# Optimization experiments

Measured on AMD Instinct MI355X. Metric: run time of the kernel, lower is better.

Reference implementation:

```python
import jax, jax.numpy as jnp
import numpy as np

N = 50000
E_RAND = 800000
IN, HID, OUT = 128, 64, 40
HEADS = (2, 1, 1)
NEG_SLOPE = 0.2


def setup_inputs() -> dict:
    key = jax.random.key(0)
    ks = jax.random.split(key, 16)
    # random edges with src != dst, then append self-loops (remove+add_self_loop)
    src_r = jax.random.randint(ks[0], (E_RAND,), 0, N)
    off = jax.random.randint(ks[1], (E_RAND,), 1, N)
    dst_r = (src_r + off) % N
    loops = jnp.arange(N)
    src = jnp.concatenate([src_r, loops]).astype(jnp.int64)
    dst = jnp.concatenate([dst_r, loops]).astype(jnp.int64)
    in_feat = jax.random.normal(ks[2], (N, IN), dtype=jnp.float32)

    def lin(k, fan_in, fan_out):
        return jax.random.normal(k, (fan_in, fan_out), dtype=jnp.float32) / np.sqrt(fan_in)

    H0, H1, H2 = HEADS
    # layer 0: in=IN, out=HID, heads=H0
    W0 = lin(ks[3], IN, H0 * HID)
    al0 = jax.random.normal(ks[4], (H0, HID), dtype=jnp.float32) * 0.1
    ar0 = jax.random.normal(ks[5], (H0, HID), dtype=jnp.float32) * 0.1
    b0 = jnp.zeros((H0 * HID,), dtype=jnp.float32)
    # layer 1: in=HID*H0, out=HID, heads=H1
    W1 = lin(ks[6], HID * H0, H1 * HID)
    al1 = jax.random.normal(ks[7], (H1, HID), dtype=jnp.float32) * 0.1
    ar1 = jax.random.normal(ks[8], (H1, HID), dtype=jnp.float32) * 0.1
    b1 = jnp.zeros((H1 * HID,), dtype=jnp.float32)
    # layer 2: in=HID*H1, out=OUT, heads=H2
    W2 = lin(ks[9], HID * H1, H2 * OUT)
    al2 = jax.random.normal(ks[10], (H2, OUT), dtype=jnp.float32) * 0.1
    ar2 = jax.random.normal(ks[11], (H2, OUT), dtype=jnp.float32) * 0.1
    b2 = jnp.zeros((H2 * OUT,), dtype=jnp.float32)
    return {"in_feat": in_feat, "src": src, "dst": dst,
            "W0": W0, "al0": al0, "ar0": ar0, "b0": b0,
            "W1": W1, "al1": al1, "ar1": ar1, "b1": b1,
            "W2": W2, "al2": al2, "ar2": ar2, "b2": b2}


def _gat_layer(x, src, dst, W, al, ar, b):
    # x: [N, Fin]; W: [Fin, H*D]; al/ar: [H, D]; b: [H*D]
    H, D = al.shape
    feat = (x @ W).reshape(-1, H, D)                 # [N, H, D]
    el = jnp.sum(feat * al, axis=-1)                 # [N, H]
    er = jnp.sum(feat * ar, axis=-1)                 # [N, H]
    e = jax.nn.leaky_relu(el[src] + er[dst], NEG_SLOPE)  # [E, H]
    m = jax.ops.segment_max(e, dst, num_segments=x.shape[0])
    ee = jnp.exp(e - jax.lax.stop_gradient(m)[dst])
    s = jax.ops.segment_sum(ee, dst, num_segments=x.shape[0])
    alpha = ee / s[dst]                              # softmax over in-edges per dst
    out = jax.ops.segment_sum(feat[src] * alpha[:, :, None], dst,
                              num_segments=x.shape[0])  # [N, H, D]
    return out + b.reshape(1, H, D)


def reference(in_feat, src, dst, W0, al0, ar0, b0, W1, al1, ar1, b1, W2, al2, ar2, b2):
    h = _gat_layer(in_feat, src, dst, W0, al0, ar0, b0).reshape(in_feat.shape[0], -1)  # flatten(1)
    h = _gat_layer(h, src, dst, W1, al1, ar1, b1).mean(axis=1)                          # mean over heads
    h = _gat_layer(h, src, dst, W2, al2, ar2, b2).reshape(in_feat.shape[0], -1)         # flatten(1)
    return h
```

## Files before the change

kernel.cpp:

```cpp
#include <hip/hip_runtime.h>
#include <hip/hip_fp16.h>
#include <math.h>

#define NEG_SLOPE 0.2f


__device__ inline float2 up2(unsigned u) {
    __half2 h;
    __builtin_memcpy(&h, &u, 4);
    return __half22float2(h);
}
__device__ inline unsigned pk2(float a, float b) {
    __half2 h = __floats2half2_rn(a, b);
    unsigned u;
    __builtin_memcpy(&u, &h, 4);
    return u;
}
__device__ inline void fma8(float* acc, const uint4& v, float p) {
    float2 f;
    f = up2(v.x); acc[0] += f.x * p; acc[1] += f.y * p;
    f = up2(v.y); acc[2] += f.x * p; acc[3] += f.y * p;
    f = up2(v.z); acc[4] += f.x * p; acc[5] += f.y * p;
    f = up2(v.w); acc[6] += f.x * p; acc[7] += f.y * p;
}
__device__ inline void fma4(float4& a, const float4& w, float xs) {
    a.x += w.x * xs; a.y += w.y * xs; a.z += w.z * xs; a.w += w.w * xs;
}
__device__ inline float dot4(const float4& a, const float4& b) {
    return a.x * b.x + a.y * b.y + a.z * b.z + a.w * b.w;
}


__global__ __launch_bounds__(256) void degree_hist_rank(const int* __restrict__ dst,
                                                        int* __restrict__ deg,
                                                        int* __restrict__ rank, int E) {
    int e = blockIdx.x * blockDim.x + threadIdx.x;
    if (e < E) rank[e] = atomicAdd(&deg[dst[e]], 1);
}

__global__ __launch_bounds__(256) void scan_block_sums(const int* __restrict__ in,
                                                       int* __restrict__ partial, int n) {
    int i = blockIdx.x * 256 + threadIdx.x;
    int v = (i < n) ? in[i] : 0;
#pragma unroll
    for (int off = 32; off; off >>= 1) v += __shfl_xor(v, off);
    __shared__ int wsum[4];
    if ((threadIdx.x & 63) == 0) wsum[threadIdx.x >> 6] = v;
    __syncthreads();
    if (threadIdx.x == 0) partial[blockIdx.x] = wsum[0] + wsum[1] + wsum[2] + wsum[3];
}

__global__ __launch_bounds__(256) void scan_offsets(const int* __restrict__ partial,
                                                    int* __restrict__ partial_scan,
                                                    int* __restrict__ total_out, int nb,
                                                    const float* __restrict__ W2,
                                                    const float* __restrict__ al2,
                                                    const float* __restrict__ ar2,
                                                    float* __restrict__ W2p,
                                                    float* __restrict__ al2p,
                                                    float* __restrict__ ar2p) {
    __shared__ int buf[256];
    int t = threadIdx.x;
    int v = (t < nb) ? partial[t] : 0;
    buf[t] = v;
    __syncthreads();
    for (int off = 1; off < 256; off <<= 1) {
        int x = (t >= off) ? buf[t - off] : 0;
        __syncthreads();
        buf[t] += x;
        __syncthreads();
    }
    partial_scan[t] = buf[t] - v;
    if (t == 255) *total_out = buf[255];
    for (int i = t; i < 64 * 64; i += 256) {
        int r = i >> 6, c = i & 63;
        W2p[i] = (c < 40) ? W2[r * 40 + c] : 0.f;
    }
    if (t < 64) {
        al2p[t] = (t < 40) ? al2[t] : 0.f;
        ar2p[t] = (t < 40) ? ar2[t] : 0.f;
    }
}

__global__ __launch_bounds__(256) void scan_final(const int* __restrict__ in,
                                                  const int* __restrict__ partial_scan,
                                                  int* __restrict__ out, int n) {
    __shared__ int buf[256];
    int t = threadIdx.x;
    int i = blockIdx.x * 256 + t;
    int v = (i < n) ? in[i] : 0;
    buf[t] = v;
    __syncthreads();
    for (int off = 1; off < 256; off <<= 1) {
        int x = (t >= off) ? buf[t - off] : 0;
        __syncthreads();
        buf[t] += x;
        __syncthreads();
    }
    if (i < n) out[i] = partial_scan[blockIdx.x] + buf[t] - v;
}

__global__ __launch_bounds__(256) void scatter_rank(const int* __restrict__ src,
                                                    const int* __restrict__ dst,
                                                    const int* __restrict__ rank,
                                                    const int* __restrict__ row_start,
                                                    int* __restrict__ csr_src, int E) {
    int e = blockIdx.x * blockDim.x + threadIdx.x;
    if (e >= E) return;
    int d = dst[e];
    csr_src[row_start[d] + rank[e]] = src[e];
}


template <int K, int M, int G, int RPG, int H, int FSTRIDE>
__global__ __launch_bounds__((M / 4) * G) void gemm_feat_lds(const float* __restrict__ x,
                                                             const float* __restrict__ W,
                                                             const float* __restrict__ al,
                                                             const float* __restrict__ ar,
                                                             __half* __restrict__ outh,
                                                             float* __restrict__ el,
                                                             float* __restrict__ er, int N) {
    constexpr int CT = M / 4;
    constexpr int NT = CT * G;
    constexpr int ROWS = G * RPG;
    constexpr int KC = 32;
    constexpr int KC4 = KC / 4;
    constexpr int NCH = K / KC;
    constexpr int LPH = 16;
    static_assert(CT % LPH == 0, "CT must be a multiple of 16");
    __shared__ float4 sx[ROWS][KC4 + 1];
    __shared__ float4 sw[KC][CT];
    const int tid = threadIdx.x;
    const int col4 = tid % CT;
    const int grp = tid / CT;
    const int h = col4 / LPH;
    const float4* __restrict__ W4 = (const float4*)W;
    const float4* __restrict__ x4 = (const float4*)x;
    const float4 av = ((const float4*)al)[col4];
    const float4 rv = ((const float4*)ar)[col4];

    for (int base = blockIdx.x * ROWS; base < N; base += gridDim.x * ROWS) {
        float4 acc[RPG];
#pragma unroll
        for (int rr = 0; rr < RPG; ++rr) acc[rr] = float4{0.f, 0.f, 0.f, 0.f};

        for (int ch = 0; ch < NCH; ++ch) {
            __syncthreads();
#pragma unroll
            for (int i = tid; i < KC * CT; i += NT)
                sw[i / CT][i % CT] = W4[(size_t)(ch * KC) * CT + i];
#pragma unroll
            for (int i = tid; i < ROWS * KC4; i += NT) {
                int r = i / KC4, c = i % KC4;
                int row = base + r;
                sx[r][c] = (row < N) ? x4[(size_t)row * (K / 4) + ch * KC4 + c]
                                     : float4{0.f, 0.f, 0.f, 0.f};
            }
            __syncthreads();
#pragma unroll
            for (int k4 = 0; k4 < KC4; ++k4) {
                float4 w0 = sw[4 * k4 + 0][col4];
                float4 w1 = sw[4 * k4 + 1][col4];
                float4 w2 = sw[4 * k4 + 2][col4];
                float4 w3 = sw[4 * k4 + 3][col4];
#pragma unroll
                for (int rr = 0; rr < RPG; ++rr) {
                    float4 xv = sx[grp * RPG + rr][k4];
                    fma4(acc[rr], w0, xv.x);
                    fma4(acc[rr], w1, xv.y);
                    fma4(acc[rr], w2, xv.z);
                    fma4(acc[rr], w3, xv.w);
                }
            }
        }
#pragma unroll
        for (int rr = 0; rr < RPG; ++rr) {
            int row = base + grp * RPG + rr;
            if (row < N) {
                uint2 pkd;
                pkd.x = pk2(acc[rr].x, acc[rr].y);
                pkd.y = pk2(acc[rr].z, acc[rr].w);
                ((uint2*)(outh + (size_t)row * FSTRIDE))[col4] = pkd;
            }
        }
#pragma unroll
        for (int rr = 0; rr < RPG; ++rr) {
            float pl = dot4(acc[rr], av);
            float pr = dot4(acc[rr], rv);
#pragma unroll
            for (int off = 1; off < LPH; off <<= 1) {
                pl += __shfl_xor(pl, off);
                pr += __shfl_xor(pr, off);
            }
            if ((col4 % LPH) == 0) {
                int row = base + grp * RPG + rr;
                if (row < N) {
                    el[(size_t)row * H + h] = pl;
                    er[(size_t)row * H + h] = pr;
                }
            }
        }
    }
}


template <int H, int D, int FSTRIDE, int T>
__global__ __launch_bounds__(256) void gat_aggregate(const __half* __restrict__ feat,
                                                     const float* __restrict__ el,
                                                     const float* __restrict__ er,
                                                     const int* __restrict__ row_start,
                                                     const int* __restrict__ csr_src,
                                                     const float* __restrict__ bias,
                                                     float* __restrict__ out, int N) {
    constexpr int NLp = FSTRIDE / 8;
    constexpr int Gn = 64 / NLp;
    constexpr int BATCH = Gn * T;
    constexpr int WL = (H * D) / 8;
    static_assert(BATCH <= 64 && 64 % NLp == 0, "layout");
    int dstn = (blockIdx.x * blockDim.x + threadIdx.x) >> 6;
    int lane = threadIdx.x & 63;
    if (dstn >= N) return;
    int beg = row_start[dstn], end = row_start[dstn + 1];
    int cnt = end - beg;

    float er_d[H];
#pragma unroll
    for (int h = 0; h < H; ++h) er_d[h] = er[(size_t)dstn * H + h];

    float ssum[H];
    float acc8[8];
#pragma unroll
    for (int h = 0; h < H; ++h) ssum[h] = 0.f;
#pragma unroll
    for (int i = 0; i < 8; ++i) acc8[i] = 0.f;

    const int g = lane / NLp;
    const int ln = lane % NLp;

    auto gather = [&](int s_reg, const float p_reg[H], int j) {
        uint4 v[T];
#pragma unroll
        for (int t = 0; t < T; ++t) {
            int sj = __shfl(s_reg, j + Gn * t + g);
            v[t] = ((const uint4*)(feat + (size_t)sj * FSTRIDE))[ln];
        }
#pragma unroll
        for (int t = 0; t < T; ++t) {
            int slot = j + Gn * t + g;
            float pj = __shfl(p_reg[0], slot);
            if constexpr (H == 2) {
                float pj1 = __shfl(p_reg[1], slot);
                pj = (ln >= 8) ? pj1 : pj;
            }
            fma8(acc8, v[t], pj);
        }
    };

    if (cnt <= 64) {
        int idx = beg + lane;
        bool valid = idx < end;
        int s = valid ? csr_src[idx] : csr_src[beg];
        float ev[H], m[H], p[H];
        if constexpr (H == 2) {
            float2 e2 = ((const float2*)el)[s];
            ev[0] = e2.x + er_d[0];
            ev[1] = e2.y + er_d[1];
        } else {
            ev[0] = el[s] + er_d[0];
        }
#pragma unroll
        for (int h = 0; h < H; ++h) {
            float e = ev[h];
            e = (e > 0.f) ? e : NEG_SLOPE * e;
            ev[h] = e;
            m[h] = valid ? e : -INFINITY;
        }
#pragma unroll
        for (int h = 0; h < H; ++h)
#pragma unroll
            for (int off = 32; off; off >>= 1) m[h] = fmaxf(m[h], __shfl_xor(m[h], off));
#pragma unroll
        for (int h = 0; h < H; ++h) {
            p[h] = valid ? expf(ev[h] - m[h]) : 0.f;
            ssum[h] = p[h];
        }
        for (int j = 0; j < cnt; j += BATCH) gather(s, p, j);
    } else {
        float m[H];
#pragma unroll
        for (int h = 0; h < H; ++h) m[h] = -INFINITY;
        for (int i = beg + lane; i < end; i += 64) {
            int s = csr_src[i];
            float ev[H];
            if constexpr (H == 2) {
                float2 e2 = ((const float2*)el)[s];
                ev[0] = e2.x + er_d[0];
                ev[1] = e2.y + er_d[1];
            } else {
                ev[0] = el[s] + er_d[0];
            }
#pragma unroll
            for (int h = 0; h < H; ++h) {
                float e = ev[h];
                e = (e > 0.f) ? e : NEG_SLOPE * e;
                m[h] = fmaxf(m[h], e);
            }
        }
#pragma unroll
        for (int h = 0; h < H; ++h)
#pragma unroll
            for (int off = 32; off; off >>= 1) m[h] = fmaxf(m[h], __shfl_xor(m[h], off));

        for (int base = beg; base < end; base += 64) {
            int idx = base + lane;
            bool valid = idx < end;
            int s = valid ? csr_src[idx] : csr_src[beg];
            float p[H];
            float ev[H];
            if constexpr (H == 2) {
                float2 e2 = ((const float2*)el)[s];
                ev[0] = e2.x + er_d[0];
                ev[1] = e2.y + er_d[1];
            } else {
                ev[0] = el[s] + er_d[0];
            }
#pragma unroll
            for (int h = 0; h < H; ++h) {
                float e = ev[h];
                e = (e > 0.f) ? e : NEG_SLOPE * e;
                p[h] = valid ? expf(e - m[h]) : 0.f;
                ssum[h] += p[h];
            }
            int ccnt = (end - base < 64) ? end - base : 64;
            for (int j = 0; j < ccnt; j += BATCH) gather(s, p, j);
        }
    }

#pragma unroll
    for (int h = 0; h < H; ++h)
#pragma unroll
        for (int off = 32; off; off >>= 1) ssum[h] += __shfl_xor(ssum[h], off);
#pragma unroll
    for (int i = 0; i < 8; ++i) {
#pragma unroll
        for (int off = NLp; off < 64; off <<= 1) acc8[i] += __shfl_xor(acc8[i], off);
    }
    if (lane < WL) {
        float inv;
        if constexpr (H == 2) inv = 1.f / ((lane >= 8) ? ssum[1] : ssum[0]);
        else inv = 1.f / ssum[0];
        float4* op = (float4*)(out + (size_t)dstn * (H * D));
        const float4* bp = (const float4*)bias;
        float4 bv0 = bp[2 * lane], bv1 = bp[2 * lane + 1];
        float4 o0, o1;
        o0.x = acc8[0] * inv + bv0.x; o0.y = acc8[1] * inv + bv0.y;
        o0.z = acc8[2] * inv + bv0.z; o0.w = acc8[3] * inv + bv0.w;
        o1.x = acc8[4] * inv + bv1.x; o1.y = acc8[5] * inv + bv1.y;
        o1.z = acc8[6] * inv + bv1.z; o1.w = acc8[7] * inv + bv1.w;
        op[2 * lane] = o0;
        op[2 * lane + 1] = o1;
    }
}


extern "C" void kernel_launch(void* const* d_in, const int* in_sizes, int n_in,
                              void* d_out, int out_size, void* d_ws, size_t ws_size,
                              hipStream_t stream) {
    const float* in_feat = (const float*)d_in[0];
    const int*   src     = (const int*)d_in[1];
    const int*   dst     = (const int*)d_in[2];
    const float* W0 = (const float*)d_in[3];
    const float* al0 = (const float*)d_in[4];
    const float* ar0 = (const float*)d_in[5];
    const float* b0 = (const float*)d_in[6];
    const float* W1 = (const float*)d_in[7];
    const float* al1 = (const float*)d_in[8];
    const float* ar1 = (const float*)d_in[9];
    const float* b1 = (const float*)d_in[10];
    const float* W2 = (const float*)d_in[11];
    const float* al2 = (const float*)d_in[12];
    const float* ar2 = (const float*)d_in[13];
    const float* b2 = (const float*)d_in[14];
    float* out = (float*)d_out;

    const int N = in_sizes[0] / 128;
    const int E = in_sizes[1];

    char* ws = (char*)d_ws;
    auto alloc = [&](size_t bytes) -> void* {
        void* p = (void*)ws;
        ws += (bytes + 255) & ~(size_t)255;
        return p;
    };
    int* deg       = (int*)alloc((size_t)N * 4);
    int* row_start = (int*)alloc((size_t)(N + 1) * 4);
    int* csr_src   = (int*)alloc((size_t)E * 4);
    int* rank      = (int*)alloc((size_t)E * 4);
    int* partial      = (int*)alloc(256 * 4);
    int* partial_scan = (int*)alloc(256 * 4);
    __half* feat   = (__half*)alloc((size_t)N * 128 * 2);
    float* el      = (float*)alloc((size_t)N * 2 * 4);
    float* er      = (float*)alloc((size_t)N * 2 * 4);
    float* h0      = (float*)alloc((size_t)N * 128 * 4);
    float* h1      = (float*)alloc((size_t)N * 64 * 4);
    float* W2p     = (float*)alloc((size_t)64 * 64 * 4);
    float* al2p    = (float*)alloc(64 * 4);
    float* ar2p    = (float*)alloc(64 * 4);

    hipMemsetAsync(deg, 0, (size_t)N * 4, stream);

    int egrid = (E + 255) / 256;
    int nb = (N + 255) / 256;

    degree_hist_rank<<<egrid, 256, 0, stream>>>(dst, deg, rank, E);
    scan_block_sums<<<nb, 256, 0, stream>>>(deg, partial, N);
    scan_offsets<<<1, 256, 0, stream>>>(partial, partial_scan, &row_start[N], nb,
                                        W2, al2, ar2, W2p, al2p, ar2p);
    scan_final<<<nb, 256, 0, stream>>>(deg, partial_scan, row_start, N);
    scatter_rank<<<egrid, 256, 0, stream>>>(src, dst, rank, row_start, csr_src, E);

    int ngrid = (N * 64 + 255) / 256;
    int ggrid32 = (N + 31) / 32;
    int ggrid64 = (N + 63) / 64;

    gemm_feat_lds<128, 128, 8, 4, 2, 128><<<ggrid32, 256, 0, stream>>>(in_feat, W0, al0, ar0, feat, el, er, N);
    gat_aggregate<2, 64, 128, 4><<<ngrid, 256, 0, stream>>>(feat, el, er, row_start, csr_src, b0, h0, N);

    gemm_feat_lds<128, 64, 16, 4, 1, 64><<<ggrid64, 256, 0, stream>>>(h0, W1, al1, ar1, feat, el, er, N);
    gat_aggregate<1, 64, 64, 4><<<ngrid, 256, 0, stream>>>(feat, el, er, row_start, csr_src, b1, h1, N);

    gemm_feat_lds<64, 64, 16, 4, 1, 64><<<ggrid64, 256, 0, stream>>>(h1, W2p, al2p, ar2p, feat, el, er, N);
    gat_aggregate<1, 40, 64, 4><<<ngrid, 256, 0, stream>>>(feat, el, er, row_start, csr_src, b2, out, N);
}
```

Before: 311.3 us.

## Drop softmax max-subtraction, use fast exp, guard gather tail, nontemporal CSR loads

```diff
diff --git a/kernel.cpp b/kernel.cpp
--- a/kernel.cpp
+++ b/kernel.cpp
@@ -35,7 +35,10 @@
                                                         int* __restrict__ deg,
                                                         int* __restrict__ rank, int E) {
     int e = blockIdx.x * blockDim.x + threadIdx.x;
-    if (e < E) rank[e] = atomicAdd(&deg[dst[e]], 1);
+    if (e >= E) return;
+    int d = __builtin_nontemporal_load(&dst[e]);
+    int r = atomicAdd(&deg[d], 1);
+    __builtin_nontemporal_store(r, &rank[e]);
 }
 
 __global__ __launch_bounds__(256) void scan_block_sums(const int* __restrict__ in,
@@ -107,8 +110,10 @@
                                                     int* __restrict__ csr_src, int E) {
     int e = blockIdx.x * blockDim.x + threadIdx.x;
     if (e >= E) return;
-    int d = dst[e];
-    csr_src[row_start[d] + rank[e]] = src[e];
+    int d = __builtin_nontemporal_load(&dst[e]);
+    int s = __builtin_nontemporal_load(&src[e]);
+    int r = __builtin_nontemporal_load(&rank[e]);
+    csr_src[row_start[d] + r] = s;
 }
 
 
@@ -237,22 +242,26 @@
     const int g = lane / NLp;
     const int ln = lane % NLp;
 
-    auto gather = [&](int s_reg, const float p_reg[H], int j) {
+    auto gather = [&](int s_reg, const float p_reg[H], int j, int limit) {
         uint4 v[T];
 #pragma unroll
         for (int t = 0; t < T; ++t) {
-            int sj = __shfl(s_reg, j + Gn * t + g);
-            v[t] = ((const uint4*)(feat + (size_t)sj * FSTRIDE))[ln];
+            if (j + Gn * t < limit) {
+                int sj = __shfl(s_reg, j + Gn * t + g);
+                v[t] = ((const uint4*)(feat + (size_t)sj * FSTRIDE))[ln];
+            }
         }
 #pragma unroll
         for (int t = 0; t < T; ++t) {
-            int slot = j + Gn * t + g;
-            float pj = __shfl(p_reg[0], slot);
-            if constexpr (H == 2) {
-                float pj1 = __shfl(p_reg[1], slot);
-                pj = (ln >= 8) ? pj1 : pj;
-            }
-            fma8(acc8, v[t], pj);
+            if (j + Gn * t < limit) {
+                int slot = j + Gn * t + g;
+                float pj = __shfl(p_reg[0], slot);
+                if constexpr (H == 2) {
+                    float pj1 = __shfl(p_reg[1], slot);
+                    pj = (ln >= 8) ? pj1 : pj;
+                }
+                fma8(acc8, v[t], pj);
+            }
         }
     };
 
@@ -260,7 +269,7 @@
         int idx = beg + lane;
         bool valid = idx < end;
         int s = valid ? csr_src[idx] : csr_src[beg];
-        float ev[H], m[H], p[H];
+        float ev[H], p[H];
         if constexpr (H == 2) {
             float2 e2 = ((const float2*)el)[s];
             ev[0] = e2.x + er_d[0];
@@ -272,45 +281,11 @@
         for (int h = 0; h < H; ++h) {
             float e = ev[h];
             e = (e > 0.f) ? e : NEG_SLOPE * e;
-            ev[h] = e;
-            m[h] = valid ? e : -INFINITY;
-        }
-#pragma unroll
-        for (int h = 0; h < H; ++h)
-#pragma unroll
-            for (int off = 32; off; off >>= 1) m[h] = fmaxf(m[h], __shfl_xor(m[h], off));
-#pragma unroll
-        for (int h = 0; h < H; ++h) {
-            p[h] = valid ? expf(ev[h] - m[h]) : 0.f;
+            p[h] = valid ? __expf(e) : 0.f;
             ssum[h] = p[h];
         }
-        for (int j = 0; j < cnt; j += BATCH) gather(s, p, j);
+        for (int j = 0; j < cnt; j += BATCH) gather(s, p, j, cnt);
     } else {
-        float m[H];
-#pragma unroll
-        for (int h = 0; h < H; ++h) m[h] = -INFINITY;
-        for (int i = beg + lane; i < end; i += 64) {
-            int s = csr_src[i];
-            float ev[H];
-            if constexpr (H == 2) {
-                float2 e2 = ((const float2*)el)[s];
-                ev[0] = e2.x + er_d[0];
-                ev[1] = e2.y + er_d[1];
-            } else {
-                ev[0] = el[s] + er_d[0];
-            }
-#pragma unroll
-            for (int h = 0; h < H; ++h) {
-                float e = ev[h];
-                e = (e > 0.f) ? e : NEG_SLOPE * e;
-                m[h] = fmaxf(m[h], e);
-            }
-        }
-#pragma unroll
-        for (int h = 0; h < H; ++h)
-#pragma unroll
-            for (int off = 32; off; off >>= 1) m[h] = fmaxf(m[h], __shfl_xor(m[h], off));
-
         for (int base = beg; base < end; base += 64) {
             int idx = base + lane;
             bool valid = idx < end;
@@ -328,11 +303,11 @@
             for (int h = 0; h < H; ++h) {
                 float e = ev[h];
                 e = (e > 0.f) ? e : NEG_SLOPE * e;
-                p[h] = valid ? expf(e - m[h]) : 0.f;
+                p[h] = valid ? __expf(e) : 0.f;
                 ssum[h] += p[h];
             }
             int ccnt = (end - base < 64) ? end - base : 64;
-            for (int j = 0; j < ccnt; j += BATCH) gather(s, p, j);
+            for (int j = 0; j < ccnt; j += BATCH) gather(s, p, j, ccnt);
         }
     }
 
```

Measured after the change: 308.6 us. No clear change (-0.9%).
